# Performance work log

Measured on AMD Instinct MI355X. Metric: run time of the kernel, lower is better.

## Reference

```python
import jax, jax.numpy as jnp
import numpy as np

D_MODEL = 1024
N_HEADS = 16
D_HEAD = D_MODEL // N_HEADS
SCALE = 1.0 / np.sqrt(D_HEAD).astype(np.float32)


def _feature_map(x):
    # phi(x) = elu(x) + 1
    return jax.nn.elu(x) + 1.0


def setup_inputs() -> dict:
    key = jax.random.key(0)
    ks = jax.random.split(key, 7)
    b, s = 4, 2048
    w = 1.0 / np.sqrt(D_MODEL).astype(np.float32)
    return {
        "x": jax.random.normal(ks[0], (b, s, D_MODEL), dtype=jnp.float32),
        "Wq": jax.random.normal(ks[1], (D_MODEL, D_MODEL), dtype=jnp.float32) * w,
        "Wk": jax.random.normal(ks[2], (D_MODEL, D_MODEL), dtype=jnp.float32) * w,
        "Wv": jax.random.normal(ks[3], (D_MODEL, D_MODEL), dtype=jnp.float32) * w,
        "Wo": jax.random.normal(ks[4], (D_MODEL, D_MODEL), dtype=jnp.float32) * w,
        "Wg": jax.random.normal(ks[5], (N_HEADS, D_MODEL), dtype=jnp.float32) * w,
        "bg": jax.random.normal(ks[6], (N_HEADS,), dtype=jnp.float32) * 0.02,
    }


def reference(x, Wq, Wk, Wv, Wo, Wg, bg):
    b, s, _ = x.shape
    # projections (PyTorch Linear: y = x @ W.T)
    q = (x @ Wq.T).reshape(b, s, N_HEADS, D_HEAD)
    k = (x @ Wk.T).reshape(b, s, N_HEADS, D_HEAD)
    v = (x @ Wv.T).reshape(b, s, N_HEADS, D_HEAD)
    q = _feature_map(q * SCALE)
    k = _feature_map(k)
    gate = jax.nn.sigmoid(x @ Wg.T + bg)  # [b, s, h]

    # time-major for scan: [s, b, h, dh] and [s, b, h]
    qt = jnp.moveaxis(q, 1, 0)
    kt = jnp.moveaxis(k, 1, 0)
    vt = jnp.moveaxis(v, 1, 0)
    gt = jnp.moveaxis(gate, 1, 0)

    S0 = jnp.zeros((b, N_HEADS, D_HEAD, D_HEAD), dtype=x.dtype)

    def step(S, inp):
        q_t, k_t, v_t, g_t = inp
        # S_t = g_t * S_{t-1} + k_t v_t^T
        S = g_t[:, :, None, None] * S + k_t[..., :, None] * v_t[..., None, :]
        y_t = jnp.einsum("bhi,bhij->bhj", q_t, S)
        return S, y_t

    _, ys = jax.lax.scan(step, S0, (qt, kt, vt, gt))  # ys: [s, b, h, dh]
    y = jnp.moveaxis(ys, 0, 1).reshape(b, s, D_MODEL)
    return y @ Wo.T
```

## Files before the change

### kernel.cpp

```cpp
#include <hip/hip_runtime.h>
#include <hip/hip_bf16.h>
#include <math.h>

#define BATCH 4
#define SEQ 2048
#define DMODEL 1024
#define NHEADS 16
#define DHEAD 64
#define MTOK (BATCH * SEQ)
#define SCALE_Q 0.125f
#define NCHAIN (BATCH * NHEADS)
#define CT 64
#define NC (SEQ / CT)
#define SP 72
#define QKVS 3072

typedef unsigned short ushort_t;
typedef __attribute__((ext_vector_type(8))) short bf16x8;
typedef __attribute__((ext_vector_type(4))) float f32x4;

__device__ __forceinline__ float bf2f(unsigned short u) {
    return __uint_as_float(((unsigned)u) << 16);
}
__device__ __forceinline__ unsigned short f2bf(float f) {
    unsigned u = __float_as_uint(f);
    return (unsigned short)((u + 0x7fffu + ((u >> 16) & 1u)) >> 16);
}

__global__ __launch_bounds__(256) void cvt_all(const float* __restrict__ x,
                                               const float* __restrict__ Wq,
                                               const float* __restrict__ Wk,
                                               const float* __restrict__ Wv,
                                               const float* __restrict__ Wo,
                                               const float* __restrict__ Wg,
                                               const float* __restrict__ bg,
                                               ushort_t* __restrict__ xb,
                                               ushort_t* __restrict__ wcat,
                                               float* __restrict__ gate) {
    const int blk = blockIdx.x;
    const int tid = threadIdx.x;

    if (blk < MTOK) {
        const int m = blk;
        const float* xr = x + (size_t)m * DMODEL;
        {
            float4 v = ((const float4*)xr)[tid];
            ushort4 o;
            o.x = f2bf(v.x); o.y = f2bf(v.y); o.z = f2bf(v.z); o.w = f2bf(v.w);
            ((ushort4*)(xb + (size_t)m * DMODEL))[tid] = o;
        }
        const int h = tid >> 4;
        const int r = tid & 15;
        const float* wr = Wg + (size_t)h * DMODEL;
        float p = 0.f;
#pragma unroll
        for (int i = 0; i < 16; ++i) {
            const int k = (r << 2) + (i << 6);
            float4 xv = *(const float4*)&xr[k];
            float4 wv = *(const float4*)&wr[k];
            p += xv.x * wv.x + xv.y * wv.y + xv.z * wv.z + xv.w * wv.w;
        }
        p += __shfl_xor(p, 8, 64);
        p += __shfl_xor(p, 4, 64);
        p += __shfl_xor(p, 2, 64);
        p += __shfl_xor(p, 1, 64);
        if (r == 0) {
            float vv = p + bg[h];
            gate[(size_t)m * NHEADS + h] = 1.f / (1.f + __expf(-vv));
        }
    } else {
        const int row = blk - MTOK;
        const float* src;
        if (row < 1024)      src = Wq + (size_t)row * DMODEL;
        else if (row < 2048) src = Wk + (size_t)(row - 1024) * DMODEL;
        else if (row < 3072) src = Wv + (size_t)(row - 2048) * DMODEL;
        else                 src = Wo + (size_t)(row - 3072) * DMODEL;
        float4 v = ((const float4*)src)[tid];
        ushort4 o;
        o.x = f2bf(v.x); o.y = f2bf(v.y); o.z = f2bf(v.z); o.w = f2bf(v.w);
        ((ushort4*)(wcat + (size_t)row * DMODEL))[tid] = o;
    }
}

#define GT 128
#define GBK 32

__global__ __launch_bounds__(256) void gemm_bf16(const ushort_t* __restrict__ A,
                                                 const ushort_t* __restrict__ B,
                                                 float* __restrict__ Cf,
                                                 ushort_t* __restrict__ Cb,
                                                 int M, int N, int K,
                                                 int mode) {
    __shared__ ushort_t As[2][GT * GBK];
    __shared__ ushort_t Bs[2][GT * GBK];

    const int tid = threadIdx.x;
    const int w = tid >> 6;
    const int l = tid & 63;
    const int m0 = blockIdx.y * GT;
    const int n0 = blockIdx.x * GT;
    const int wm = (w >> 1) * 64;
    const int wn = (w & 1) * 64;

    const int srow = l >> 2;
    const int schunk = ((l & 3) ^ ((l >> 3) & 3)) * 8;

    const ushort_t* aseg[2];
    const ushort_t* bseg[2];
#pragma unroll
    for (int i = 0; i < 2; ++i) {
        const int s = w * 2 + i;
        aseg[i] = A + (size_t)(m0 + s * 16 + srow) * K + schunk;
        bseg[i] = B + (size_t)(n0 + s * 16 + srow) * K + schunk;
    }

#define STAGE(buf, k0)                                                          \
    do {                                                                        \
        _Pragma("unroll")                                                       \
        for (int i_ = 0; i_ < 2; ++i_) {                                        \
            const int s_ = w * 2 + i_;                                          \
            __builtin_amdgcn_global_load_lds(                                   \
                (const __attribute__((address_space(1))) unsigned int*)(const void*)(aseg[i_] + (k0)), \
                (__attribute__((address_space(3))) unsigned int*)(void*)&As[buf][s_ * 16 * GBK], \
                16, 0, 0);                                                      \
            __builtin_amdgcn_global_load_lds(                                   \
                (const __attribute__((address_space(1))) unsigned int*)(const void*)(bseg[i_] + (k0)), \
                (__attribute__((address_space(3))) unsigned int*)(void*)&Bs[buf][s_ * 16 * GBK], \
                16, 0, 0);                                                      \
        }                                                                       \
    } while (0)

    f32x4 acc[4][4];
#pragma unroll
    for (int i = 0; i < 4; ++i)
#pragma unroll
        for (int j = 0; j < 4; ++j)
#pragma unroll
            for (int r = 0; r < 4; ++r) acc[i][j][r] = 0.f;

    const int fr = l & 15;
    const int fsw = (((l >> 4) ^ ((fr >> 1) & 3))) * 8;

    STAGE(0, 0);

    const int nit = K / GBK;
    for (int it = 0; it < nit; ++it) {
        __syncthreads();
        if (it + 1 < nit) STAGE((it + 1) & 1, (it + 1) * GBK);

        const ushort_t* __restrict__ as = As[it & 1];
        const ushort_t* __restrict__ bs = Bs[it & 1];

        bf16x8 af[4], bfr[4];
#pragma unroll
        for (int ti = 0; ti < 4; ++ti)
            af[ti] = *(const bf16x8*)&as[(wm + ti * 16 + fr) * GBK + fsw];
#pragma unroll
        for (int tj = 0; tj < 4; ++tj)
            bfr[tj] = *(const bf16x8*)&bs[(wn + tj * 16 + fr) * GBK + fsw];
#pragma unroll
        for (int ti = 0; ti < 4; ++ti)
#pragma unroll
            for (int tj = 0; tj < 4; ++tj)
                acc[ti][tj] = __builtin_amdgcn_mfma_f32_16x16x32_bf16(
                    af[ti], bfr[tj], acc[ti][tj], 0, 0, 0);
    }
#undef STAGE

    float escale = 1.0f;
    bool do_phi = false;
    if (mode == 3) {
        do_phi = (n0 < 2048);
        escale = (n0 < 1024) ? SCALE_Q : 1.0f;
    }

    const int er = (l >> 4) * 4;
    const int ec = l & 15;
#pragma unroll
    for (int ti = 0; ti < 4; ++ti)
#pragma unroll
        for (int tj = 0; tj < 4; ++tj)
#pragma unroll
            for (int r = 0; r < 4; ++r) {
                const int row = m0 + wm + ti * 16 + er + r;
                const int col = n0 + wn + tj * 16 + ec;
                float val = acc[ti][tj][r];
                if (mode == 0) {
                    Cf[(size_t)row * N + col] = val;
                } else {
                    val *= escale;
                    if (do_phi) val = (val > 0.f) ? (val + 1.f) : __expf(val);
                    Cb[(size_t)row * N + col] = f2bf(val);
                }
            }
}

__global__ __launch_bounds__(256) void p1_kernel(const ushort_t* __restrict__ qkv,
                                                 const float* __restrict__ gate,
                                                 float* __restrict__ Dt,
                                                 float* __restrict__ Bg) {
    const int tile = blockIdx.x;
    const int chain = tile >> 5;
    const int c = tile & 31;
    const int b = chain >> 4;
    const int h = chain & 15;
    const int tid = threadIdx.x;
    const int w = tid >> 6;
    const int l = tid & 63;

    __shared__ ushort_t Kt[DHEAD * SP];
    __shared__ ushort_t Vt[DHEAD * SP];
    __shared__ float bs[CT];

    const int tau = tid >> 2;
    const int seg = (tid & 3) * 16;
    const size_t grow = ((size_t)(b * SEQ + c * CT + tau)) * QKVS + h * DHEAD + seg;
    union { float4 f4[2]; ushort_t us[16]; } uk, uv;
    uk.f4[0] = *(const float4*)&qkv[grow + 1024];
    uk.f4[1] = *(const float4*)&qkv[grow + 1024 + 8];
    uv.f4[0] = *(const float4*)&qkv[grow + 2048];
    uv.f4[1] = *(const float4*)&qkv[grow + 2048 + 8];

    if (tid < 64) {
        float g = gate[((size_t)(b * SEQ + c * CT + tid)) * NHEADS + h];
        float lg = __logf(g);
#pragma unroll
        for (int d = 1; d < 64; d <<= 1) {
            float n = __shfl_up(lg, d, 64);
            if (l >= d) lg += n;
        }
        bs[tid] = lg;
        if (tid == 63) Bg[tile] = lg;
    }
    __syncthreads();

    const float e = __expf(bs[63] - bs[tau]);
#pragma unroll
    for (int f = 0; f < 16; ++f) {
        Kt[(seg + f) * SP + tau] = f2bf(e * bf2f(uk.us[f]));
        Vt[(seg + f) * SP + tau] = uv.us[f];
    }
    __syncthreads();

    const int fr = l & 15;
    const int fq = (l >> 4) * 8;
    const int jw = w * 16;

    f32x4 accD[4];
#pragma unroll
    for (int nt = 0; nt < 4; ++nt)
#pragma unroll
        for (int r = 0; r < 4; ++r) accD[nt][r] = 0.f;

#pragma unroll
    for (int kc = 0; kc < 2; ++kc) {
        bf16x8 va = *(const bf16x8*)&Vt[(jw + fr) * SP + kc * 32 + fq];
#pragma unroll
        for (int nt = 0; nt < 4; ++nt) {
            bf16x8 kf = *(const bf16x8*)&Kt[(nt * 16 + fr) * SP + kc * 32 + fq];
            accD[nt] = __builtin_amdgcn_mfma_f32_16x16x32_bf16(va, kf, accD[nt], 0, 0, 0);
        }
    }

    const int er = (l >> 4) * 4;
    const size_t dbase = (size_t)tile * (DHEAD * DHEAD);
#pragma unroll
    for (int nt = 0; nt < 4; ++nt)
#pragma unroll
        for (int r = 0; r < 4; ++r) {
            const int j = jw + er + r;
            const int i = nt * 16 + fr;
            Dt[dbase + j * DHEAD + i] = accD[nt][r];
        }
}

__global__ __launch_bounds__(256) void p2_kernel(const float* __restrict__ Dt,
                                                 const float* __restrict__ Bg,
                                                 ushort_t* __restrict__ St) {
    const int chain = blockIdx.x >> 2;
    const int jq = (blockIdx.x & 3) * 16;
    const int tid = threadIdx.x;
    const int jj = jq + (tid >> 4);
    const int ii = (tid & 15) * 4;

    float4 S = make_float4(0.f, 0.f, 0.f, 0.f);
    for (int c = 0; c < NC; ++c) {
        const size_t base = (((size_t)chain * NC + c) * DHEAD + jj) * DHEAD + ii;
        ushort4 o;
        o.x = f2bf(S.x); o.y = f2bf(S.y); o.z = f2bf(S.z); o.w = f2bf(S.w);
        *(ushort4*)&St[base] = o;
        const float eB = __expf(Bg[chain * NC + c]);
        const float4 D = *(const float4*)&Dt[base];
        S.x = eB * S.x + D.x;
        S.y = eB * S.y + D.y;
        S.z = eB * S.z + D.z;
        S.w = eB * S.w + D.w;
    }
}

__global__ __launch_bounds__(256) void p3_kernel(const ushort_t* __restrict__ qkv,
                                                 const ushort_t* __restrict__ St,
                                                 const float* __restrict__ gate,
                                                 ushort_t* __restrict__ yb) {
    const int tile = blockIdx.x;
    const int chain = tile >> 5;
    const int c = tile & 31;
    const int b = chain >> 4;
    const int h = chain & 15;
    const int tid = threadIdx.x;
    const int w = tid >> 6;
    const int l = tid & 63;

    __shared__ ushort_t Qs[CT * SP];
    __shared__ ushort_t Ks[CT * SP];
    __shared__ ushort_t Vt[DHEAD * SP];
    __shared__ ushort_t Ss[CT * SP];
    __shared__ ushort_t Ps[CT * SP];
    __shared__ float bs[CT];

    {
        const int row = tid >> 2;
        const int seg = (tid & 3) * 16;
        const size_t grow = ((size_t)(b * SEQ + c * CT + row)) * QKVS + h * DHEAD + seg;
        float4 q0 = *(const float4*)&qkv[grow];
        float4 q1 = *(const float4*)&qkv[grow + 8];
        float4 k0 = *(const float4*)&qkv[grow + 1024];
        float4 k1 = *(const float4*)&qkv[grow + 1024 + 8];
        union { float4 f4[2]; ushort_t us[16]; } uv;
        uv.f4[0] = *(const float4*)&qkv[grow + 2048];
        uv.f4[1] = *(const float4*)&qkv[grow + 2048 + 8];
        const size_t srow = (((size_t)chain * NC + c) * DHEAD + row) * DHEAD + seg;
        float4 s0 = *(const float4*)&St[srow];
        float4 s1 = *(const float4*)&St[srow + 8];
        *(float4*)&Qs[row * SP + seg]     = q0;
        *(float4*)&Qs[row * SP + seg + 8] = q1;
        *(float4*)&Ks[row * SP + seg]     = k0;
        *(float4*)&Ks[row * SP + seg + 8] = k1;
        *(float4*)&Ss[row * SP + seg]     = s0;
        *(float4*)&Ss[row * SP + seg + 8] = s1;
#pragma unroll
        for (int f = 0; f < 16; ++f)
            Vt[(seg + f) * SP + row] = uv.us[f];
    }
    if (tid < 64) {
        float g = gate[((size_t)(b * SEQ + c * CT + tid)) * NHEADS + h];
        float lg = __logf(g);
#pragma unroll
        for (int d = 1; d < 64; d <<= 1) {
            float n = __shfl_up(lg, d, 64);
            if (l >= d) lg += n;
        }
        bs[tid] = lg;
    }
    __syncthreads();

    const int fr = l & 15;
    const int fq = (l >> 4) * 8;
    const int tw = w * 16;

    bf16x8 qa[2];
#pragma unroll
    for (int kc = 0; kc < 2; ++kc)
        qa[kc] = *(const bf16x8*)&Qs[(tw + fr) * SP + kc * 32 + fq];

    f32x4 accA[4], accP[4];
#pragma unroll
    for (int nt = 0; nt < 4; ++nt)
#pragma unroll
        for (int r = 0; r < 4; ++r) { accA[nt][r] = 0.f; accP[nt][r] = 0.f; }

#pragma unroll
    for (int kc = 0; kc < 2; ++kc)
#pragma unroll
        for (int nt = 0; nt < 4; ++nt) {
            bf16x8 sb = *(const bf16x8*)&Ss[(nt * 16 + fr) * SP + kc * 32 + fq];
            accA[nt] = __builtin_amdgcn_mfma_f32_16x16x32_bf16(qa[kc], sb, accA[nt], 0, 0, 0);
            bf16x8 kf = *(const bf16x8*)&Ks[(nt * 16 + fr) * SP + kc * 32 + fq];
            accP[nt] = __builtin_amdgcn_mfma_f32_16x16x32_bf16(qa[kc], kf, accP[nt], 0, 0, 0);
        }

    const int er = (l >> 4) * 4;
    int trow[4];
    float bt[4];
#pragma unroll
    for (int r = 0; r < 4; ++r) { trow[r] = tw + er + r; bt[r] = bs[trow[r]]; }
#pragma unroll
    for (int nt = 0; nt < 4; ++nt) {
        const int tau = nt * 16 + fr;
        const float btau = bs[tau];
#pragma unroll
        for (int r = 0; r < 4; ++r) {
            float f = (tau <= trow[r]) ? __expf(bt[r] - btau) : 0.f;
            Ps[trow[r] * SP + tau] = f2bf(accP[nt][r] * f);
        }
    }

    f32x4 accY[4];
#pragma unroll
    for (int r = 0; r < 4; ++r) {
        const float eb = __expf(bt[r]);
#pragma unroll
        for (int nt = 0; nt < 4; ++nt) accY[nt][r] = accA[nt][r] * eb;
    }
#pragma unroll
    for (int kc = 0; kc < 2; ++kc) {
        bf16x8 pa = *(const bf16x8*)&Ps[(tw + fr) * SP + kc * 32 + fq];
#pragma unroll
        for (int nt = 0; nt < 4; ++nt) {
            bf16x8 vf = *(const bf16x8*)&Vt[(nt * 16 + fr) * SP + kc * 32 + fq];
            accY[nt] = __builtin_amdgcn_mfma_f32_16x16x32_bf16(pa, vf, accY[nt], 0, 0, 0);
        }
    }

    const size_t ybase = ((size_t)(b * SEQ + c * CT)) * DMODEL + h * DHEAD;
#pragma unroll
    for (int nt = 0; nt < 4; ++nt)
#pragma unroll
        for (int r = 0; r < 4; ++r)
            yb[ybase + (size_t)trow[r] * DMODEL + nt * 16 + fr] = f2bf(accY[nt][r]);
}

extern "C" void kernel_launch(void* const* d_in, const int* in_sizes, int n_in,
                              void* d_out, int out_size, void* d_ws, size_t ws_size,
                              hipStream_t stream) {
    const float* x  = (const float*)d_in[0];
    const float* Wq = (const float*)d_in[1];
    const float* Wk = (const float*)d_in[2];
    const float* Wv = (const float*)d_in[3];
    const float* Wo = (const float*)d_in[4];
    const float* Wg = (const float*)d_in[5];
    const float* bg = (const float*)d_in[6];
    float* out = (float*)d_out;

    const size_t elems = (size_t)MTOK * DMODEL;
    const size_t welems = (size_t)DMODEL * DMODEL;
    const size_t stelems = (size_t)NCHAIN * NC * DHEAD * DHEAD;

    ushort_t* xb   = (ushort_t*)d_ws;
    ushort_t* St   = xb;
    ushort_t* qkv  = xb + elems;
    ushort_t* wcat = qkv + (size_t)MTOK * QKVS;
    float* gate    = (float*)(wcat + 4 * welems);
    float* Bg      = gate + (size_t)MTOK * NHEADS;
    float* Dt      = Bg + (size_t)NCHAIN * NC;
    ushort_t* yb   = (ushort_t*)Dt;

    const size_t need = (size_t)((char*)(Dt + stelems) - (char*)d_ws);
    if (ws_size < need) return;

    cvt_all<<<dim3(MTOK + 4096), dim3(256), 0, stream>>>(x, Wq, Wk, Wv, Wo, Wg, bg,
                                                         xb, wcat, gate);

    gemm_bf16<<<dim3(QKVS / GT, MTOK / GT), dim3(256), 0, stream>>>(
        xb, wcat, nullptr, qkv, MTOK, QKVS, DMODEL, 3);

    p1_kernel<<<dim3(NCHAIN * NC), dim3(256), 0, stream>>>(qkv, gate, Dt, Bg);
    p2_kernel<<<dim3(NCHAIN * 4), dim3(256), 0, stream>>>(Dt, Bg, St);
    p3_kernel<<<dim3(NCHAIN * NC), dim3(256), 0, stream>>>(qkv, St, gate, yb);

    gemm_bf16<<<dim3(DMODEL / GT, MTOK / GT), dim3(256), 0, stream>>>(
        yb, wcat + 3 * welems, out, nullptr, MTOK, DMODEL, DMODEL, 0);
}
```

Measured before the change: 267.2 us.

## Fold gate projection into QKV GEMM and remap tiles for L2 locality

The sigmoid gate projection moves out of the conversion kernel. Wg is padded to 128 rows and appended to the QKV weight matrix, so the fused GEMM computes the gate in an extra column tile and applies bias and sigmoid in its epilogue. The GEMM launch also switches to a flat 1-D grid with a grouped tile remapping meant to improve L2 reuse. This removes the scalar fp32 dot-product work from the conversion pass. The cost is a mostly-zero extra GEMM tile column and gate values now computed from bf16 inputs instead of fp32.

```diff
diff --git a/kernel.cpp b/kernel.cpp
--- a/kernel.cpp
+++ b/kernel.cpp
@@ -14,6 +14,7 @@
 #define NC (SEQ / CT)
 #define SP 72
 #define QKVS 3072
+#define WROWS 4224
 
 typedef unsigned short ushort_t;
 typedef __attribute__((ext_vector_type(8))) short bf16x8;
@@ -33,51 +34,32 @@
                                                const float* __restrict__ Wv,
                                                const float* __restrict__ Wo,
                                                const float* __restrict__ Wg,
-                                               const float* __restrict__ bg,
                                                ushort_t* __restrict__ xb,
-                                               ushort_t* __restrict__ wcat,
-                                               float* __restrict__ gate) {
+                                               ushort_t* __restrict__ wcat) {
     const int blk = blockIdx.x;
     const int tid = threadIdx.x;
 
     if (blk < MTOK) {
-        const int m = blk;
-        const float* xr = x + (size_t)m * DMODEL;
-        {
-            float4 v = ((const float4*)xr)[tid];
-            ushort4 o;
-            o.x = f2bf(v.x); o.y = f2bf(v.y); o.z = f2bf(v.z); o.w = f2bf(v.w);
-            ((ushort4*)(xb + (size_t)m * DMODEL))[tid] = o;
-        }
-        const int h = tid >> 4;
-        const int r = tid & 15;
-        const float* wr = Wg + (size_t)h * DMODEL;
-        float p = 0.f;
-#pragma unroll
-        for (int i = 0; i < 16; ++i) {
-            const int k = (r << 2) + (i << 6);
-            float4 xv = *(const float4*)&xr[k];
-            float4 wv = *(const float4*)&wr[k];
-            p += xv.x * wv.x + xv.y * wv.y + xv.z * wv.z + xv.w * wv.w;
-        }
-        p += __shfl_xor(p, 8, 64);
-        p += __shfl_xor(p, 4, 64);
-        p += __shfl_xor(p, 2, 64);
-        p += __shfl_xor(p, 1, 64);
-        if (r == 0) {
-            float vv = p + bg[h];
-            gate[(size_t)m * NHEADS + h] = 1.f / (1.f + __expf(-vv));
-        }
+        const float* xr = x + (size_t)blk * DMODEL;
+        float4 v = ((const float4*)xr)[tid];
+        ushort4 o;
+        o.x = f2bf(v.x); o.y = f2bf(v.y); o.z = f2bf(v.z); o.w = f2bf(v.w);
+        ((ushort4*)(xb + (size_t)blk * DMODEL))[tid] = o;
     } else {
         const int row = blk - MTOK;
-        const float* src;
-        if (row < 1024)      src = Wq + (size_t)row * DMODEL;
-        else if (row < 2048) src = Wk + (size_t)(row - 1024) * DMODEL;
-        else if (row < 3072) src = Wv + (size_t)(row - 2048) * DMODEL;
-        else                 src = Wo + (size_t)(row - 3072) * DMODEL;
-        float4 v = ((const float4*)src)[tid];
         ushort4 o;
-        o.x = f2bf(v.x); o.y = f2bf(v.y); o.z = f2bf(v.z); o.w = f2bf(v.w);
+        if (row >= 3088 && row < 3200) {
+            o.x = o.y = o.z = o.w = 0;
+        } else {
+            const float* src;
+            if (row < 1024)      src = Wq + (size_t)row * DMODEL;
+            else if (row < 2048) src = Wk + (size_t)(row - 1024) * DMODEL;
+            else if (row < 3072) src = Wv + (size_t)(row - 2048) * DMODEL;
+            else if (row < 3088) src = Wg + (size_t)(row - 3072) * DMODEL;
+            else                 src = Wo + (size_t)(row - 3200) * DMODEL;
+            float4 v = ((const float4*)src)[tid];
+            o.x = f2bf(v.x); o.y = f2bf(v.y); o.z = f2bf(v.z); o.w = f2bf(v.w);
+        }
         ((ushort4*)(wcat + (size_t)row * DMODEL))[tid] = o;
     }
 }
@@ -89,6 +71,8 @@
                                                  const ushort_t* __restrict__ B,
                                                  float* __restrict__ Cf,
                                                  ushort_t* __restrict__ Cb,
+                                                 float* __restrict__ gatep,
+                                                 const float* __restrict__ bgp,
                                                  int M, int N, int K,
                                                  int mode) {
     __shared__ ushort_t As[2][GT * GBK];
@@ -97,8 +81,15 @@
     const int tid = threadIdx.x;
     const int w = tid >> 6;
     const int l = tid & 63;
-    const int m0 = blockIdx.y * GT;
-    const int n0 = blockIdx.x * GT;
+
+    const int flat = blockIdx.x;
+    const int kx = flat & 7;
+    const int ii = flat >> 3;
+    const int bx = ii >> 3;
+    const int by = (kx << 3) | (ii & 7);
+    const int m0 = by * GT;
+    const int n0 = bx * GT;
+
     const int wm = (w >> 1) * 64;
     const int wn = (w & 1) * 64;
 
@@ -167,6 +158,23 @@
     }
 #undef STAGE
 
+    const int er = (l >> 4) * 4;
+    const int ec = l & 15;
+
+    if (mode == 3 && n0 == 3072) {
+#pragma unroll
+        for (int ti = 0; ti < 4; ++ti)
+#pragma unroll
+            for (int r = 0; r < 4; ++r) {
+                if (wn == 0) {
+                    const int row = m0 + wm + ti * 16 + er + r;
+                    const float vv = acc[ti][0][r] + bgp[ec];
+                    gatep[(size_t)row * NHEADS + ec] = 1.f / (1.f + __expf(-vv));
+                }
+            }
+        return;
+    }
+
     float escale = 1.0f;
     bool do_phi = false;
     if (mode == 3) {
@@ -174,8 +182,6 @@
         escale = (n0 < 1024) ? SCALE_Q : 1.0f;
     }
 
-    const int er = (l >> 4) * 4;
-    const int ec = l & 15;
 #pragma unroll
     for (int ti = 0; ti < 4; ++ti)
 #pragma unroll
@@ -190,7 +196,7 @@
                 } else {
                     val *= escale;
                     if (do_phi) val = (val > 0.f) ? (val + 1.f) : __expf(val);
-                    Cb[(size_t)row * N + col] = f2bf(val);
+                    Cb[(size_t)row * QKVS + col] = f2bf(val);
                 }
             }
 }
@@ -440,7 +446,7 @@
     ushort_t* St   = xb;
     ushort_t* qkv  = xb + elems;
     ushort_t* wcat = qkv + (size_t)MTOK * QKVS;
-    float* gate    = (float*)(wcat + 4 * welems);
+    float* gate    = (float*)(wcat + (size_t)WROWS * DMODEL);
     float* Bg      = gate + (size_t)MTOK * NHEADS;
     float* Dt      = Bg + (size_t)NCHAIN * NC;
     ushort_t* yb   = (ushort_t*)Dt;
@@ -448,16 +454,16 @@
     const size_t need = (size_t)((char*)(Dt + stelems) - (char*)d_ws);
     if (ws_size < need) return;
 
-    cvt_all<<<dim3(MTOK + 4096), dim3(256), 0, stream>>>(x, Wq, Wk, Wv, Wo, Wg, bg,
-                                                         xb, wcat, gate);
-
-    gemm_bf16<<<dim3(QKVS / GT, MTOK / GT), dim3(256), 0, stream>>>(
-        xb, wcat, nullptr, qkv, MTOK, QKVS, DMODEL, 3);
+    cvt_all<<<dim3(MTOK + WROWS), dim3(256), 0, stream>>>(x, Wq, Wk, Wv, Wo, Wg, xb, wcat);
+
+    gemm_bf16<<<dim3(25 * 64), dim3(256), 0, stream>>>(
+        xb, wcat, nullptr, qkv, gate, bg, MTOK, QKVS, DMODEL, 3);
 
     p1_kernel<<<dim3(NCHAIN * NC), dim3(256), 0, stream>>>(qkv, gate, Dt, Bg);
     p2_kernel<<<dim3(NCHAIN * 4), dim3(256), 0, stream>>>(Dt, Bg, St);
     p3_kernel<<<dim3(NCHAIN * NC), dim3(256), 0, stream>>>(qkv, St, gate, yb);
 
-    gemm_bf16<<<dim3(DMODEL / GT, MTOK / GT), dim3(256), 0, stream>>>(
-        yb, wcat + 3 * welems, out, nullptr, MTOK, DMODEL, DMODEL, 0);
-}
+    gemm_bf16<<<dim3(8 * 64), dim3(256), 0, stream>>>(
+        yb, wcat + (size_t)3200 * DMODEL, out, nullptr, nullptr, nullptr,
+        MTOK, DMODEL, DMODEL, 0);
+}
```

Result: faster. 243.2 us (-9.0%).
